# Kernel optimization log

Hardware: AMD Instinct MI355X
Metric: run time of the kernel (lower is better)

The kernel has to match this reference:

```python
import jax, jax.numpy as jnp
import numpy as np

N_NODES = 100000
N_EDGES = 1600000
IN_F = 32
HID = 128


def setup_inputs() -> dict:
    key = jax.random.key(0)
    ks = jax.random.split(key, 8)
    x = jax.random.normal(ks[0], (N_NODES, IN_F), dtype=jnp.float32)
    edge_index = jax.random.randint(ks[1], (2, N_EDGES), 0, N_NODES, dtype=jnp.int64)
    # Glorot-ish scaled weights
    W1 = jax.random.normal(ks[2], (IN_F, HID), dtype=jnp.float32) / np.sqrt(IN_F)
    b1 = jnp.zeros((HID,), dtype=jnp.float32)
    W2 = jax.random.normal(ks[3], (HID, HID), dtype=jnp.float32) / np.sqrt(HID)
    b2 = jnp.zeros((HID,), dtype=jnp.float32)
    W3 = jax.random.normal(ks[4], (HID, IN_F), dtype=jnp.float32) / np.sqrt(HID)
    b3 = jnp.zeros((IN_F,), dtype=jnp.float32)
    return {"x": x, "edge_index": edge_index, "W1": W1, "b1": b1,
            "W2": W2, "b2": b2, "W3": W3, "b3": b3}


def _gcn_norm(edge_index, n_nodes):
    # Add self-loops (PyG GCNConv default) and compute symmetric normalization
    loops = jnp.arange(n_nodes, dtype=edge_index.dtype)
    src = jnp.concatenate([edge_index[0], loops])
    dst = jnp.concatenate([edge_index[1], loops])
    ones = jnp.ones(src.shape[0], dtype=jnp.float32)
    deg = jax.ops.segment_sum(ones, dst, num_segments=n_nodes)
    deg_inv_sqrt = jnp.where(deg > 0, jax.lax.rsqrt(deg), 0.0)
    norm = deg_inv_sqrt[src] * deg_inv_sqrt[dst]  # [E + N]
    return src, dst, norm


def _gcn_conv(x, src, dst, norm, W, b, n_nodes):
    h = x @ W                                # [N, out] transform first (smaller msgs when out<in)
    msg = h[src] * norm[:, None]             # gather + edge-wise scale  [E+N, out]
    out = jax.ops.segment_sum(msg, dst, num_segments=n_nodes)  # scatter-add
    return out + b


def reference(x, edge_index, W1, b1, W2, b2, W3, b3):
    n = x.shape[0]
    src, dst, norm = _gcn_norm(edge_index, n)
    h = jax.nn.relu(_gcn_conv(x, src, dst, norm, W1, b1, n))
    h = jax.nn.relu(_gcn_conv(h, src, dst, norm, W2, b2, n))
    h = jax.nn.relu(_gcn_conv(h, src, dst, norm, W3, b3, n))
    return h
```

## Files before the change

kernel.cpp:

```cpp
#include <hip/hip_runtime.h>
#include <hip/hip_fp16.h>

#define N_NODES 100000
#define N_EDGES 1600000
#define IN_F 32
#define HID 128
#define NBLK_SCAN 391
#define BSHIFT 9
#define BSIZE 512
#define NBUCK 196
#define EPB 8192
#define NBB 196

typedef _Float16 half8 __attribute__((ext_vector_type(8)));
typedef float floatx4 __attribute__((ext_vector_type(4)));

static __device__ __forceinline__ void pack2(_Float16* dst, float a, float b) {
    union { _Float16 h[2]; unsigned u; } p;
    p.h[0] = (_Float16)a; p.h[1] = (_Float16)b;
    *(unsigned*)dst = p.u;
}


__global__ void k_zero_ideg(int* __restrict__ ideg) {
    int i = blockIdx.x * 256 + threadIdx.x;
    if (i < N_NODES) ideg[i] = 0;
}

__global__ void k_count(const int* __restrict__ dst, int* __restrict__ ideg) {
    int e = blockIdx.x * 256 + threadIdx.x;
    if (e < N_EDGES) atomicAdd(&ideg[dst[e]], 1);
}

__global__ __launch_bounds__(256) void k_scan1(const int* __restrict__ ideg,
                                               int* __restrict__ cursor,
                                               int* __restrict__ partials) {
    __shared__ int s[256];
    int gid = blockIdx.x * 256 + threadIdx.x;
    int v = (gid < N_NODES) ? ideg[gid] : 0;
    s[threadIdx.x] = v;
    __syncthreads();
    for (int off = 1; off < 256; off <<= 1) {
        int t = (threadIdx.x >= off) ? s[threadIdx.x - off] : 0;
        __syncthreads();
        s[threadIdx.x] += t;
        __syncthreads();
    }
    if (gid < N_NODES) cursor[gid] = s[threadIdx.x] - v;
    if (threadIdx.x == 255) partials[blockIdx.x] = s[255];
}

__global__ __launch_bounds__(512) void k_scan2(int* __restrict__ partials) {
    __shared__ int s[512];
    int v = (threadIdx.x < NBLK_SCAN) ? partials[threadIdx.x] : 0;
    s[threadIdx.x] = v;
    __syncthreads();
    for (int off = 1; off < 512; off <<= 1) {
        int t = (threadIdx.x >= off) ? s[threadIdx.x - off] : 0;
        __syncthreads();
        s[threadIdx.x] += t;
        __syncthreads();
    }
    if (threadIdx.x < NBLK_SCAN) partials[threadIdx.x] = s[threadIdx.x] - v;
}

__global__ void k_scan3(int* __restrict__ cursor, const int* __restrict__ partials) {
    int gid = blockIdx.x * 256 + threadIdx.x;
    if (gid < N_NODES) cursor[gid] += partials[blockIdx.x];
}

__global__ void k_binit(const int* __restrict__ cursor, int* __restrict__ bcur) {
    int t = threadIdx.x;
    if (t < NBUCK) bcur[t] = cursor[t << BSHIFT];
}

__global__ __launch_bounds__(256) void k_bucket(const int* __restrict__ src,
                                                const int* __restrict__ dst,
                                                int* __restrict__ bcur,
                                                unsigned* __restrict__ rec) {
    __shared__ int hist[256];
    __shared__ int lbase[256];
    const int e0 = blockIdx.x * EPB;
    hist[threadIdx.x] = 0;
    __syncthreads();

    unsigned rk[32]; short bk[32];
#pragma unroll
    for (int k = 0; k < 32; ++k) {
        int e = e0 + k * 256 + threadIdx.x;
        if (e < N_EDGES) {
            int d = dst[e];
            int b = d >> BSHIFT;
            bk[k] = (short)b;
            rk[k] = ((unsigned)src[e] << BSHIFT) | (unsigned)(d & (BSIZE - 1));
            atomicAdd(&hist[b], 1);
        } else bk[k] = -1;
    }
    __syncthreads();
    int c = hist[threadIdx.x];
    lbase[threadIdx.x] = (c > 0) ? atomicAdd(&bcur[threadIdx.x], c) : 0;
    __syncthreads();
    hist[threadIdx.x] = 0;
    __syncthreads();
#pragma unroll
    for (int k = 0; k < 32; ++k) {
        if (bk[k] >= 0) {
            int off = atomicAdd(&hist[bk[k]], 1);
            rec[lbase[bk[k]] + off] = rk[k];
        }
    }
}

__global__ __launch_bounds__(256) void k_fill2(const int* __restrict__ cursor,
                                               const unsigned* __restrict__ rec,
                                               int* __restrict__ col) {
    __shared__ int lcur[BSIZE];
    const int b = blockIdx.x;
    const int n0 = b << BSHIFT;
    for (int t = threadIdx.x; t < BSIZE; t += 256) {
        int n = n0 + t;
        lcur[t] = (n < N_NODES) ? cursor[n] : 0;
    }
    const int rbeg = cursor[n0];
    const int rend = (b == NBUCK - 1) ? N_EDGES : cursor[n0 + BSIZE];
    __syncthreads();
    for (int i = rbeg + threadIdx.x; i < rend; i += 256) {
        unsigned r = rec[i];
        int slot = atomicAdd(&lcur[r & (BSIZE - 1)], 1);
        col[slot] = (int)(r >> BSHIFT);
    }
}


__global__ void k_prescale(const float2* __restrict__ x, const int* __restrict__ ideg,
                           __half2* __restrict__ T) {
    int tid = blockIdx.x * 256 + threadIdx.x;
    if (tid >= N_NODES * 16) return;
    int i = tid >> 4;
    float dis = rsqrtf(1.0f + (float)ideg[i]);
    float2 v = x[tid];
    T[tid] = __floats2half2_rn(v.x * dis, v.y * dis);
}


__global__ __launch_bounds__(256) void k_gather32_pre(
    const int* __restrict__ cursor, const int* __restrict__ ideg,
    const int* __restrict__ col, const _Float16* __restrict__ T,
    _Float16* __restrict__ OUT) {
    const int lane = threadIdx.x & 63;
    const int slot = lane >> 2;
    const int fl   = lane & 3;
    const int wid  = blockIdx.x * 4 + (threadIdx.x >> 6);
    const int wstride = gridDim.x * 4;

    for (int node = wid; node < N_NODES; node += wstride) {
        int begin = cursor[node];
        int d     = ideg[node];
        int end   = begin + d;
        float acc[8];
        if (slot == 0) {
            half8 v = *(const half8*)(T + (size_t)node * IN_F + fl * 8);
#pragma unroll
            for (int i = 0; i < 8; ++i) acc[i] = (float)v[i];
        } else {
#pragma unroll
            for (int i = 0; i < 8; ++i) acc[i] = 0.f;
        }
        for (int e = begin; e < end; e += 16) {
            int ee = e + slot;
            if (ee < end) {
                int s = col[ee];
                half8 v = *(const half8*)(T + (size_t)s * IN_F + fl * 8);
#pragma unroll
                for (int i = 0; i < 8; ++i) acc[i] += (float)v[i];
            }
        }
#pragma unroll
        for (int m = 4; m < 64; m <<= 1)
#pragma unroll
            for (int i = 0; i < 8; ++i) acc[i] += __shfl_xor(acc[i], m, 64);
        if (slot == 0) {
            float dis = rsqrtf(1.0f + (float)d);
            half8 o;
#pragma unroll
            for (int i = 0; i < 8; ++i) o[i] = (_Float16)(acc[i] * dis);
            *(half8*)(OUT + (size_t)node * IN_F + fl * 8) = o;
        }
    }
}

__global__ __launch_bounds__(256) void k_gather32_fin(
    const int* __restrict__ cursor, const int* __restrict__ ideg,
    const int* __restrict__ col, const _Float16* __restrict__ T,
    const float* __restrict__ b, float* __restrict__ OUT) {
    const int lane = threadIdx.x & 63;
    const int slot = lane >> 2;
    const int fl   = lane & 3;
    const int wid  = blockIdx.x * 4 + (threadIdx.x >> 6);
    const int wstride = gridDim.x * 4;

    float4 bb0 = *(const float4*)(b + fl * 8);
    float4 bb1 = *(const float4*)(b + fl * 8 + 4);
    float bias[8] = {bb0.x, bb0.y, bb0.z, bb0.w, bb1.x, bb1.y, bb1.z, bb1.w};

    for (int node = wid; node < N_NODES; node += wstride) {
        int begin = cursor[node];
        int d     = ideg[node];
        int end   = begin + d;
        float acc[8];
        if (slot == 0) {
            half8 v = *(const half8*)(T + (size_t)node * IN_F + fl * 8);
#pragma unroll
            for (int i = 0; i < 8; ++i) acc[i] = (float)v[i];
        } else {
#pragma unroll
            for (int i = 0; i < 8; ++i) acc[i] = 0.f;
        }
        for (int e = begin; e < end; e += 16) {
            int ee = e + slot;
            if (ee < end) {
                int s = col[ee];
                half8 v = *(const half8*)(T + (size_t)s * IN_F + fl * 8);
#pragma unroll
                for (int i = 0; i < 8; ++i) acc[i] += (float)v[i];
            }
        }
#pragma unroll
        for (int m = 4; m < 64; m <<= 1)
#pragma unroll
            for (int i = 0; i < 8; ++i) acc[i] += __shfl_xor(acc[i], m, 64);
        if (slot == 0) {
            float dis = rsqrtf(1.0f + (float)d);
            float o[8];
#pragma unroll
            for (int i = 0; i < 8; ++i) {
                float v = acc[i] * dis + bias[i];
                o[i] = v > 0.f ? v : 0.f;
            }
            float* op = OUT + (size_t)node * IN_F + fl * 8;
            *(float4*)op       = make_float4(o[0], o[1], o[2], o[3]);
            *(float4*)(op + 4) = make_float4(o[4], o[5], o[6], o[7]);
        }
    }
}

__global__ __launch_bounds__(256) void k_gather128(
    const int* __restrict__ cursor, const int* __restrict__ ideg,
    const int* __restrict__ col, const _Float16* __restrict__ T,
    const float* __restrict__ b, _Float16* __restrict__ OUT) {
    const int lane = threadIdx.x & 63;
    const int slot = lane >> 4;
    const int fl   = lane & 15;
    const int wid  = blockIdx.x * 4 + (threadIdx.x >> 6);
    const int wstride = gridDim.x * 4;

    float4 bb0 = *(const float4*)(b + fl * 8);
    float4 bb1 = *(const float4*)(b + fl * 8 + 4);
    float bias[8] = {bb0.x, bb0.y, bb0.z, bb0.w, bb1.x, bb1.y, bb1.z, bb1.w};

    for (int node = wid; node < N_NODES; node += wstride) {
        int begin = cursor[node];
        int d     = ideg[node];
        int end   = begin + d;
        float acc[8];
        if (slot == 0) {
            half8 v = *(const half8*)(T + (size_t)node * HID + fl * 8);
#pragma unroll
            for (int i = 0; i < 8; ++i) acc[i] = (float)v[i];
        } else {
#pragma unroll
            for (int i = 0; i < 8; ++i) acc[i] = 0.f;
        }
        for (int e = begin; e < end; e += 8) {
            int ee0 = e + slot;
            int ee1 = e + 4 + slot;
            if (ee1 < end) {
                int s0 = col[ee0];
                int s1 = col[ee1];
                half8 v0 = *(const half8*)(T + (size_t)s0 * HID + fl * 8);
                half8 v1 = *(const half8*)(T + (size_t)s1 * HID + fl * 8);
#pragma unroll
                for (int i = 0; i < 8; ++i) acc[i] += (float)v0[i] + (float)v1[i];
            } else if (ee0 < end) {
                int s0 = col[ee0];
                half8 v0 = *(const half8*)(T + (size_t)s0 * HID + fl * 8);
#pragma unroll
                for (int i = 0; i < 8; ++i) acc[i] += (float)v0[i];
            }
        }
#pragma unroll
        for (int m = 16; m < 64; m <<= 1)
#pragma unroll
            for (int i = 0; i < 8; ++i) acc[i] += __shfl_xor(acc[i], m, 64);
        if (slot == 0) {
            float dis = rsqrtf(1.0f + (float)d);
            half8 o;
#pragma unroll
            for (int i = 0; i < 8; ++i) {
                float v = acc[i] * dis + bias[i];
                o[i] = (_Float16)(v > 0.f ? v : 0.f);
            }
            *(half8*)(OUT + (size_t)node * HID + fl * 8) = o;
        }
    }
}


__global__ __launch_bounds__(256) void k_xform1_mfma(
    const _Float16* __restrict__ z, const float* __restrict__ W,
    const float* __restrict__ bias, _Float16* __restrict__ Hh) {
    __shared__ _Float16 Wt[128 * 40];
    for (int idx = threadIdx.x; idx < 2048; idx += 256) {
        int n = idx & 127, k = (idx >> 7) * 2;
        pack2(&Wt[n * 40 + k], W[k * HID + n], W[(k + 1) * HID + n]);
    }
    __syncthreads();

    const int lane = threadIdx.x & 63;
    const int wave = threadIdx.x >> 6;
    const int m16 = lane & 15, quad = lane >> 4;
    const int row0 = blockIdx.x * 64 + wave * 16;
    if (row0 >= N_NODES) return;

    int arow = row0 + m16; if (arow >= N_NODES) arow = N_NODES - 1;
    half8 a = *(const half8*)(z + (size_t)arow * IN_F + quad * 8);

    floatx4 acc[8];
#pragma unroll
    for (int t = 0; t < 8; ++t) acc[t] = (floatx4){0.f, 0.f, 0.f, 0.f};
#pragma unroll
    for (int t = 0; t < 8; ++t) {
        half8 b = *(const half8*)&Wt[(t * 16 + m16) * 40 + quad * 8];
        acc[t] = __builtin_amdgcn_mfma_f32_16x16x32_f16(a, b, acc[t], 0, 0, 0);
    }
#pragma unroll
    for (int t = 0; t < 8; ++t) {
        int c = t * 16 + m16;
        float bj = bias[c];
#pragma unroll
        for (int r = 0; r < 4; ++r) {
            int row = row0 + quad * 4 + r;
            if (row < N_NODES) {
                float v = acc[t][r] + bj;
                Hh[(size_t)row * HID + c] = (_Float16)(v > 0.f ? v : 0.f);
            }
        }
    }
}

__global__ __launch_bounds__(256) void k_xform2_mfma(
    const _Float16* __restrict__ H, const float* __restrict__ W,
    const int* __restrict__ ideg, _Float16* __restrict__ T) {
    __shared__ _Float16 Wt[128 * 136];
    for (int idx = threadIdx.x; idx < 8192; idx += 256) {
        int n = idx & 127, k = (idx >> 7) * 2;
        pack2(&Wt[n * 136 + k], W[k * HID + n], W[(k + 1) * HID + n]);
    }
    __syncthreads();

    const int lane = threadIdx.x & 63;
    const int wave = threadIdx.x >> 6;
    const int m16 = lane & 15, quad = lane >> 4;
    const int row0 = blockIdx.x * 64 + wave * 16;
    if (row0 >= N_NODES) return;

    int arow = row0 + m16; if (arow >= N_NODES) arow = N_NODES - 1;
    const _Float16* hp = H + (size_t)arow * HID + quad * 8;
    half8 a[4];
#pragma unroll
    for (int kk = 0; kk < 4; ++kk) a[kk] = *(const half8*)(hp + kk * 32);

    floatx4 acc[8];
#pragma unroll
    for (int t = 0; t < 8; ++t) acc[t] = (floatx4){0.f, 0.f, 0.f, 0.f};
#pragma unroll
    for (int t = 0; t < 8; ++t) {
        const _Float16* wp = &Wt[(t * 16 + m16) * 136 + quad * 8];
#pragma unroll
        for (int kk = 0; kk < 4; ++kk) {
            half8 b = *(const half8*)(wp + kk * 32);
            acc[t] = __builtin_amdgcn_mfma_f32_16x16x32_f16(a[kk], b, acc[t], 0, 0, 0);
        }
    }
    float dis[4];
#pragma unroll
    for (int r = 0; r < 4; ++r) {
        int row = row0 + quad * 4 + r;
        dis[r] = (row < N_NODES) ? rsqrtf(1.0f + (float)ideg[row]) : 0.f;
    }
#pragma unroll
    for (int t = 0; t < 8; ++t) {
        int c = t * 16 + m16;
#pragma unroll
        for (int r = 0; r < 4; ++r) {
            int row = row0 + quad * 4 + r;
            if (row < N_NODES)
                T[(size_t)row * HID + c] = (_Float16)(acc[t][r] * dis[r]);
        }
    }
}

__global__ __launch_bounds__(256) void k_xform3_mfma(
    const _Float16* __restrict__ H, const float* __restrict__ W,
    const int* __restrict__ ideg, _Float16* __restrict__ T) {
    __shared__ _Float16 Wt[32 * 136];
    for (int idx = threadIdx.x; idx < 2048; idx += 256) {
        int n = idx & 31, k = (idx >> 5) * 2;
        pack2(&Wt[n * 136 + k], W[k * IN_F + n], W[(k + 1) * IN_F + n]);
    }
    __syncthreads();

    const int lane = threadIdx.x & 63;
    const int wave = threadIdx.x >> 6;
    const int m16 = lane & 15, quad = lane >> 4;
    const int row0 = blockIdx.x * 64 + wave * 16;
    if (row0 >= N_NODES) return;

    int arow = row0 + m16; if (arow >= N_NODES) arow = N_NODES - 1;
    const _Float16* hp = H + (size_t)arow * HID + quad * 8;
    half8 a[4];
#pragma unroll
    for (int kk = 0; kk < 4; ++kk) a[kk] = *(const half8*)(hp + kk * 32);

    floatx4 acc[2];
#pragma unroll
    for (int t = 0; t < 2; ++t) acc[t] = (floatx4){0.f, 0.f, 0.f, 0.f};
#pragma unroll
    for (int t = 0; t < 2; ++t) {
        const _Float16* wp = &Wt[(t * 16 + m16) * 136 + quad * 8];
#pragma unroll
        for (int kk = 0; kk < 4; ++kk) {
            half8 b = *(const half8*)(wp + kk * 32);
            acc[t] = __builtin_amdgcn_mfma_f32_16x16x32_f16(a[kk], b, acc[t], 0, 0, 0);
        }
    }
    float dis[4];
#pragma unroll
    for (int r = 0; r < 4; ++r) {
        int row = row0 + quad * 4 + r;
        dis[r] = (row < N_NODES) ? rsqrtf(1.0f + (float)ideg[row]) : 0.f;
    }
#pragma unroll
    for (int t = 0; t < 2; ++t) {
        int c = t * 16 + m16;
#pragma unroll
        for (int r = 0; r < 4; ++r) {
            int row = row0 + quad * 4 + r;
            if (row < N_NODES)
                T[(size_t)row * IN_F + c] = (_Float16)(acc[t][r] * dis[r]);
        }
    }
}


extern "C" void kernel_launch(void* const* d_in, const int* in_sizes, int n_in,
                              void* d_out, int out_size, void* d_ws, size_t ws_size,
                              hipStream_t stream) {
    const float* x  = (const float*)d_in[0];
    const int*   ei = (const int*)d_in[1];
    const float* W1 = (const float*)d_in[2];
    const float* b1 = (const float*)d_in[3];
    const float* W2 = (const float*)d_in[4];
    const float* b2 = (const float*)d_in[5];
    const float* W3 = (const float*)d_in[6];
    const float* b3 = (const float*)d_in[7];
    float* out = (float*)d_out;

    const int* src = ei;
    const int* dst = ei + N_EDGES;

    int*      ideg     = (int*)d_ws;
    int*      cursor   = ideg + 102400;
    int*      partials = cursor + 102400;
    int*      bcur     = partials + 512;
    int*      col      = bcur + 256;
    unsigned* rec      = (unsigned*)(col + N_EDGES);
    _Float16* t1h      = (_Float16*)(rec + N_EDGES);
    _Float16* z        = t1h + (size_t)N_NODES * IN_F;
    _Float16* H1h      = z + (size_t)N_NODES * IN_F;
    _Float16* T2h      = H1h + (size_t)N_NODES * HID;
    _Float16* H2h      = T2h + (size_t)N_NODES * HID;

    const int xgrid = (N_NODES + 63) / 64;

    k_zero_ideg<<<NBLK_SCAN, 256, 0, stream>>>(ideg);
    k_count<<<(N_EDGES + 255) / 256, 256, 0, stream>>>(dst, ideg);
    k_scan1<<<NBLK_SCAN, 256, 0, stream>>>(ideg, cursor, partials);
    k_scan2<<<1, 512, 0, stream>>>(partials);
    k_scan3<<<NBLK_SCAN, 256, 0, stream>>>(cursor, partials);
    k_binit<<<1, 256, 0, stream>>>(cursor, bcur);
    k_bucket<<<NBB, 256, 0, stream>>>(src, dst, bcur, rec);
    k_fill2<<<NBUCK, 256, 0, stream>>>(cursor, rec, col);

    k_prescale<<<(N_NODES * 16 + 255) / 256, 256, 0, stream>>>(
        (const float2*)x, ideg, (__half2*)t1h);
    k_gather32_pre<<<2048, 256, 0, stream>>>(cursor, ideg, col, t1h, z);
    k_xform1_mfma<<<xgrid, 256, 0, stream>>>(z, W1, b1, H1h);

    k_xform2_mfma<<<xgrid, 256, 0, stream>>>(H1h, W2, ideg, T2h);
    k_gather128<<<2048, 256, 0, stream>>>(cursor, ideg, col, T2h, b2, H2h);

    k_xform3_mfma<<<xgrid, 256, 0, stream>>>(H2h, W3, ideg, T2h);
    k_gather32_fin<<<2048, 256, 0, stream>>>(cursor, ideg, col, T2h, b3, out);
}
```

Before: 386.1 us.

## Derive CSR offsets from bucket counts and per-bucket local scans

Replaces the global per-node degree count (global atomics over all edges) and the three-stage node-level prefix scan with a coarse per-bucket histogram built in shared memory and a single-block bucket scan. Per-node degrees and CSR cursors are then computed inside the fill kernel from each bucket's records, using shared-memory atomics and a local scan. This removes several launches and the contended global atomics, but the fill kernel now reads its bucket's records twice.

```diff
diff --git a/kernel.cpp b/kernel.cpp
--- a/kernel.cpp
+++ b/kernel.cpp
@@ -5,7 +5,6 @@
 #define N_EDGES 1600000
 #define IN_F 32
 #define HID 128
-#define NBLK_SCAN 391
 #define BSHIFT 9
 #define BSIZE 512
 #define NBUCK 196
@@ -22,22 +21,31 @@
 }
 
 
-__global__ void k_zero_ideg(int* __restrict__ ideg) {
-    int i = blockIdx.x * 256 + threadIdx.x;
-    if (i < N_NODES) ideg[i] = 0;
-}
-
-__global__ void k_count(const int* __restrict__ dst, int* __restrict__ ideg) {
-    int e = blockIdx.x * 256 + threadIdx.x;
-    if (e < N_EDGES) atomicAdd(&ideg[dst[e]], 1);
-}
-
-__global__ __launch_bounds__(256) void k_scan1(const int* __restrict__ ideg,
-                                               int* __restrict__ cursor,
-                                               int* __restrict__ partials) {
+__global__ void k_zero_bcnt(int* __restrict__ bcnt) {
+    if (threadIdx.x < 256) bcnt[threadIdx.x] = 0;
+}
+
+__global__ __launch_bounds__(256) void k_bcount(const int* __restrict__ dst,
+                                                int* __restrict__ bcnt) {
+    __shared__ int hist[256];
+    hist[threadIdx.x] = 0;
+    __syncthreads();
+    const int e0 = blockIdx.x * EPB;
+#pragma unroll 4
+    for (int k = 0; k < 32; ++k) {
+        int e = e0 + k * 256 + threadIdx.x;
+        if (e < N_EDGES) atomicAdd(&hist[dst[e] >> BSHIFT], 1);
+    }
+    __syncthreads();
+    int c = hist[threadIdx.x];
+    if (c > 0) atomicAdd(&bcnt[threadIdx.x], c);
+}
+
+__global__ __launch_bounds__(256) void k_bscan(const int* __restrict__ bcnt,
+                                               int* __restrict__ bbase,
+                                               int* __restrict__ bcur) {
     __shared__ int s[256];
-    int gid = blockIdx.x * 256 + threadIdx.x;
-    int v = (gid < N_NODES) ? ideg[gid] : 0;
+    int v = (threadIdx.x < NBUCK) ? bcnt[threadIdx.x] : 0;
     s[threadIdx.x] = v;
     __syncthreads();
     for (int off = 1; off < 256; off <<= 1) {
@@ -46,32 +54,12 @@
         s[threadIdx.x] += t;
         __syncthreads();
     }
-    if (gid < N_NODES) cursor[gid] = s[threadIdx.x] - v;
-    if (threadIdx.x == 255) partials[blockIdx.x] = s[255];
-}
-
-__global__ __launch_bounds__(512) void k_scan2(int* __restrict__ partials) {
-    __shared__ int s[512];
-    int v = (threadIdx.x < NBLK_SCAN) ? partials[threadIdx.x] : 0;
-    s[threadIdx.x] = v;
-    __syncthreads();
-    for (int off = 1; off < 512; off <<= 1) {
-        int t = (threadIdx.x >= off) ? s[threadIdx.x - off] : 0;
-        __syncthreads();
-        s[threadIdx.x] += t;
-        __syncthreads();
-    }
-    if (threadIdx.x < NBLK_SCAN) partials[threadIdx.x] = s[threadIdx.x] - v;
-}
-
-__global__ void k_scan3(int* __restrict__ cursor, const int* __restrict__ partials) {
-    int gid = blockIdx.x * 256 + threadIdx.x;
-    if (gid < N_NODES) cursor[gid] += partials[blockIdx.x];
-}
-
-__global__ void k_binit(const int* __restrict__ cursor, int* __restrict__ bcur) {
-    int t = threadIdx.x;
-    if (t < NBUCK) bcur[t] = cursor[t << BSHIFT];
+    if (threadIdx.x < NBUCK) {
+        int ex = s[threadIdx.x] - v;
+        bbase[threadIdx.x] = ex;
+        bcur[threadIdx.x]  = ex;
+    }
+    if (threadIdx.x == 0) bbase[NBUCK] = N_EDGES;
 }
 
 __global__ __launch_bounds__(256) void k_bucket(const int* __restrict__ src,
@@ -111,18 +99,48 @@
     }
 }
 
-__global__ __launch_bounds__(256) void k_fill2(const int* __restrict__ cursor,
-                                               const unsigned* __restrict__ rec,
+__global__ __launch_bounds__(256) void k_fill3(const unsigned* __restrict__ rec,
+                                               const int* __restrict__ bbase,
+                                               int* __restrict__ ideg,
+                                               int* __restrict__ cursor,
                                                int* __restrict__ col) {
+    __shared__ int lcnt[BSIZE];
     __shared__ int lcur[BSIZE];
+    __shared__ int s[256];
     const int b = blockIdx.x;
     const int n0 = b << BSHIFT;
+    const int rbeg = bbase[b];
+    const int rend = bbase[b + 1];
+
+    lcnt[threadIdx.x] = 0;
+    lcnt[threadIdx.x + 256] = 0;
+    __syncthreads();
+    for (int i = rbeg + threadIdx.x; i < rend; i += 256)
+        atomicAdd(&lcnt[rec[i] & (BSIZE - 1)], 1);
+    __syncthreads();
+
+    int a0 = lcnt[2 * threadIdx.x], a1 = lcnt[2 * threadIdx.x + 1];
+    int pv = a0 + a1;
+    s[threadIdx.x] = pv;
+    __syncthreads();
+    for (int off = 1; off < 256; off <<= 1) {
+        int t = (threadIdx.x >= off) ? s[threadIdx.x - off] : 0;
+        __syncthreads();
+        s[threadIdx.x] += t;
+        __syncthreads();
+    }
+    int ex = s[threadIdx.x] - pv;
+    lcur[2 * threadIdx.x]     = rbeg + ex;
+    lcur[2 * threadIdx.x + 1] = rbeg + ex + a0;
+    __syncthreads();
+
     for (int t = threadIdx.x; t < BSIZE; t += 256) {
         int n = n0 + t;
-        lcur[t] = (n < N_NODES) ? cursor[n] : 0;
-    }
-    const int rbeg = cursor[n0];
-    const int rend = (b == NBUCK - 1) ? N_EDGES : cursor[n0 + BSIZE];
+        if (n < N_NODES) {
+            ideg[n]   = lcnt[t];
+            cursor[n] = lcur[t];
+        }
+    }
     __syncthreads();
     for (int i = rbeg + threadIdx.x; i < rend; i += 256) {
         unsigned r = rec[i];
@@ -469,28 +487,26 @@
     const int* src = ei;
     const int* dst = ei + N_EDGES;
 
-    int*      ideg     = (int*)d_ws;
-    int*      cursor   = ideg + 102400;
-    int*      partials = cursor + 102400;
-    int*      bcur     = partials + 512;
-    int*      col      = bcur + 256;
-    unsigned* rec      = (unsigned*)(col + N_EDGES);
-    _Float16* t1h      = (_Float16*)(rec + N_EDGES);
-    _Float16* z        = t1h + (size_t)N_NODES * IN_F;
-    _Float16* H1h      = z + (size_t)N_NODES * IN_F;
-    _Float16* T2h      = H1h + (size_t)N_NODES * HID;
-    _Float16* H2h      = T2h + (size_t)N_NODES * HID;
+    int*      ideg   = (int*)d_ws;
+    int*      cursor = ideg + 102400;
+    int*      bcnt   = cursor + 102400;
+    int*      bbase  = bcnt + 256;
+    int*      bcur   = bbase + 256;
+    int*      col    = bcur + 256;
+    unsigned* rec    = (unsigned*)(col + N_EDGES);
+    _Float16* t1h    = (_Float16*)(rec + N_EDGES);
+    _Float16* z      = t1h + (size_t)N_NODES * IN_F;
+    _Float16* H1h    = z + (size_t)N_NODES * IN_F;
+    _Float16* T2h    = H1h + (size_t)N_NODES * HID;
+    _Float16* H2h    = T2h + (size_t)N_NODES * HID;
 
     const int xgrid = (N_NODES + 63) / 64;
 
-    k_zero_ideg<<<NBLK_SCAN, 256, 0, stream>>>(ideg);
-    k_count<<<(N_EDGES + 255) / 256, 256, 0, stream>>>(dst, ideg);
-    k_scan1<<<NBLK_SCAN, 256, 0, stream>>>(ideg, cursor, partials);
-    k_scan2<<<1, 512, 0, stream>>>(partials);
-    k_scan3<<<NBLK_SCAN, 256, 0, stream>>>(cursor, partials);
-    k_binit<<<1, 256, 0, stream>>>(cursor, bcur);
+    k_zero_bcnt<<<1, 256, 0, stream>>>(bcnt);
+    k_bcount<<<NBB, 256, 0, stream>>>(dst, bcnt);
+    k_bscan<<<1, 256, 0, stream>>>(bcnt, bbase, bcur);
     k_bucket<<<NBB, 256, 0, stream>>>(src, dst, bcur, rec);
-    k_fill2<<<NBUCK, 256, 0, stream>>>(cursor, rec, col);
+    k_fill3<<<NBUCK, 256, 0, stream>>>(rec, bbase, ideg, cursor, col);
 
     k_prescale<<<(N_NODES * 16 + 255) / 256, 256, 0, stream>>>(
         (const float2*)x, ideg, (__half2*)t1h);
```

New measurement: 332.9 us. -13.8%, faster.
